# Performance work log

Hardware: AMD Instinct MI355X
Metric: run time of the kernel (lower is better)

The kernel has to match this reference:

```python
import jax, jax.numpy as jnp
import numpy as np

NUM_ITER = 20
EPS = 1e-8


def _conv(x, w, pad):
    # x: [N, Cin, H, W], w: [Cout, Cin, kh, kw] (cross-correlation, like torch conv2d)
    return jax.lax.conv_general_dilated(
        x, w, window_strides=(1, 1), padding=pad,
        dimension_numbers=('NCHW', 'OIHW', 'NCHW'))


def setup_inputs() -> dict:
    key = jax.random.key(0)
    x = jax.random.normal(key, (2, 4, 3, 256, 256), dtype=jnp.float32)
    return {
        'x': x,
        'lam': jnp.array([0.02], dtype=jnp.float32),
        'tau': jnp.array([0.25], dtype=jnp.float32),
        'theta': jnp.array([0.1], dtype=jnp.float32),
        'wx': jnp.array([[-1.0, 1.0, 0.0]], dtype=jnp.float32),
        'wy': jnp.array([[-1.0], [1.0], [0.0]], dtype=jnp.float32),
    }


def reference(x, lam, tau, theta, wx, wy):
    # x: [2, B, C, H, W] -> pairs of single-channel images [NB, 2, H, W]
    F, B, C, H, W = x.shape
    NB = B * C
    xx = jnp.moveaxis(x.reshape(2, NB, H, W), 0, 1)  # [NB, 2, H, W]

    dt = x.dtype
    gx = jnp.array([[-1., 0., 1.], [-2., 0., 2.], [-1., 0., 1.]], dt) / 6.0
    gy = jnp.array([[-1., -2., -1.], [0., 0., 0.], [1., 2., 1.]], dt) / 6.0
    grad_w = jnp.stack([gx, gy])[:, None]          # [2,1,3,3] image gradient (fixed)
    gxu = jnp.array([[0., 0., 0.], [0., -1., 1.], [0., 0., 0.]], dt)
    gyu = jnp.array([[0., 0., 0.], [0., -1., 0.], [0., 1., 0.]], dt)
    grad_u_w = jnp.stack([gxu, gyu])[:, None]      # [2,1,3,3] flow gradient (fixed)
    wx_k = wx[None, None]                          # [1,1,1,3] trainable divergence stencil
    wy_k = wy[None, None]                          # [1,1,3,1]

    rho_c = (xx[:, 1] - xx[:, 0])[:, None]                       # [NB,1,H,W]
    grad_im = _conv(xx[:, 1:], grad_w, [(1, 1), (1, 1)])         # [NB,2,H,W]
    norm_grad = jnp.sum(grad_im * grad_im, axis=1, keepdims=True) + EPS

    u = jnp.zeros((NB, 2, H, W), dt)
    p1 = jnp.zeros((NB, 2, H, W), dt)
    p2 = jnp.zeros((NB, 2, H, W), dt)

    tl = theta * lam       # [1]
    tt = tau / theta       # [1]

    def div(p):  # p: [NB,2,H,W] -> [NB,1,H,W]
        return (_conv(p[:, 0:1], wx_k, [(0, 0), (1, 1)]) +
                _conv(p[:, 1:2], wy_k, [(1, 1), (0, 0)]))

    def body(carry, _):
        u, p1, p2 = carry
        rho = rho_c + jnp.sum(grad_im * u, axis=1, keepdims=True)
        th = tl * norm_grad
        v = u - jnp.where(jnp.abs(rho) < th,
                          rho * grad_im / norm_grad,
                          tl * grad_im * jnp.sign(rho))
        u0 = v[:, 0] + theta * div(p1)[:, 0]
        u1 = v[:, 1] + theta * div(p2)[:, 0]
        u = jnp.stack([u0, u1], axis=1)
        g1 = _conv(u[:, 0:1], grad_u_w, [(1, 1), (1, 1)])
        g2 = _conv(u[:, 1:2], grad_u_w, [(1, 1), (1, 1)])
        p1 = (p1 + tt * g1) / (1.0 + tt * jnp.sum(jnp.abs(g1), axis=1, keepdims=True))
        p2 = (p2 + tt * g2) / (1.0 + tt * jnp.sum(jnp.abs(g2), axis=1, keepdims=True))
        return (u, p1, p2), None

    (u, p1, p2), _ = jax.lax.scan(body, (u, p1, p2), None, length=NUM_ITER)
    return u.reshape(B, C, 2, H, W)
```

## Files before the change

kernel.cpp:

```cpp
#include <hip/hip_runtime.h>

#define W 256
#define H 256
#define HW (W*H)
#define NB 12
#define ROWS 16
#define BPI (H/ROWS)
#define NBLK (NB*BPI)
#define NTHREADS 1024
#define NUM_ITER 20
#define TVEPS 1e-8f
#define HPLANES 8
#define FLAG_MAGIC 0x5A170000


__device__ __forceinline__ float aload(const float* p) {
    return __hip_atomic_load(p, __ATOMIC_RELAXED, __HIP_MEMORY_SCOPE_AGENT);
}
__device__ __forceinline__ void astore(float* p, float v) {
    __hip_atomic_store(p, v, __ATOMIC_RELAXED, __HIP_MEMORY_SCOPE_AGENT);
}
__device__ __forceinline__ void waitflag(const int* f, int tgt) {
    while (__hip_atomic_load(f, __ATOMIC_RELAXED, __HIP_MEMORY_SCOPE_AGENT) != tgt)
        __builtin_amdgcn_s_sleep(1);
    asm volatile("" ::: "memory");
}
__device__ __forceinline__ void setflag(int* f, int tgt) {
    asm volatile("s_waitcnt vmcnt(0)" ::: "memory");
    __hip_atomic_store(f, tgt, __ATOMIC_RELAXED, __HIP_MEMORY_SCOPE_AGENT);
}
__device__ __forceinline__ float fastrcp(float x) { return __builtin_amdgcn_rcpf(x); }

#define LD4(dst, ptr) { const float4 _t = *reinterpret_cast<const float4*>(ptr); \
                        dst[0]=_t.x; dst[1]=_t.y; dst[2]=_t.z; dst[3]=_t.w; }
#define ST4(ptr, src) { float4 _t; _t.x=src[0]; _t.y=src[1]; _t.z=src[2]; _t.w=src[3]; \
                        *reinterpret_cast<float4*>(ptr) = _t; }

__global__ __launch_bounds__(NTHREADS, 1) void tvl1_r5r_kernel(
    const float* __restrict__ xin,
    const float* __restrict__ lam,
    const float* __restrict__ tau,
    const float* __restrict__ theta,
    const float* __restrict__ wxv,
    const float* __restrict__ wyv,
    float* __restrict__ uout,
    float* __restrict__ halo,
    int* __restrict__ flags)
{
    __shared__ float xu0[ROWS+1][W];
    __shared__ float xu1[ROWS+1][W];
    __shared__ float xq1[ROWS][W];
    __shared__ float xq2[ROWS][W];

    const int tid  = threadIdx.x;
    const int lane = tid & 63;
    const int wv   = tid >> 6;
    const int x0   = lane << 2;
    const int b    = blockIdx.x;
    const int n    = b / BPI, bi = b % BPI;
    const int r0   = bi * ROWS;
    const int grow = r0 + wv;
    const bool notTop = (bi > 0), notBot = (bi < BPI-1);

    const float th0 = theta[0];
    const float tl  = th0 * lam[0];
    const float tt  = tau[0] / th0;
    const float wx0 = wxv[0], wx1 = wxv[1], wx2 = wxv[2];
    const float wy0 = wyv[0], wy1 = wyv[1], wy2 = wyv[2];

    const float* __restrict__ I0 = xin + (size_t)n * HW;
    const float* __restrict__ I1 = xin + (size_t)(NB + n) * HW;

    auto grad4 = [&](int row, float* rr, float* ggx, float* ggy) {
        #pragma unroll
        for (int c = 0; c < 4; ++c) {
            const int xc = x0 + c;
            const int idx = row * W + xc;
            const bool xm = xc > 0, xp = xc < W-1, ym = row > 0, yp = row < H-1;
            float a00=0.f,a01=0.f,a02=0.f,a10=0.f,a12=0.f,a20=0.f,a21=0.f,a22=0.f;
            if (ym) { a01=I1[idx-W]; if (xm) a00=I1[idx-W-1]; if (xp) a02=I1[idx-W+1]; }
            if (xm) a10=I1[idx-1];
            if (xp) a12=I1[idx+1];
            if (yp) { a21=I1[idx+W]; if (xm) a20=I1[idx+W-1]; if (xp) a22=I1[idx+W+1]; }
            ggx[c] = ((a02-a00) + 2.f*(a12-a10) + (a22-a20)) * (1.f/6.f);
            ggy[c] = ((a20-a00) + 2.f*(a21-a01) + (a22-a02)) * (1.f/6.f);
            rr[c]  = I1[idx] - I0[idx];
        }
    };

    float rho[4], gxr[4], gyr[4];
    grad4(grow, rho, gxr, gyr);
    float rho16[4]={0,0,0,0}, gx16[4]={0,0,0,0}, gy16[4]={0,0,0,0};
    if (wv == 14 && notBot) grad4(r0 + ROWS, rho16, gx16, gy16);

    for (int k = tid; k < (ROWS+1)*W; k += NTHREADS) { (&xu0[0][0])[k]=0.f; (&xu1[0][0])[k]=0.f; }
    for (int k = tid; k < ROWS*W;     k += NTHREADS) { (&xq1[0][0])[k]=0.f; (&xq2[0][0])[k]=0.f; }
    float u0[4]={0,0,0,0}, u1[4]={0,0,0,0};
    float p1x[4]={0,0,0,0}, p1y[4]={0,0,0,0}, p2x[4]={0,0,0,0}, p2y[4]={0,0,0,0};
    __syncthreads();

    auto ustep4 = [&](const float* rr, const float* ggx, const float* ggy,
                      const float* uu0, const float* uu1,
                      const float* x1m, const float* x1c, const float* x1p,
                      const float* q1m, const float* q1c, const float* q1p,
                      const float* x2m, const float* x2c, const float* x2p,
                      const float* q2m, const float* q2c, const float* q2p,
                      float* o0, float* o1) {
        #pragma unroll
        for (int c = 0; c < 4; ++c) {
            const float r  = rr[c] + ggx[c]*uu0[c] + ggy[c]*uu1[c];
            const float ng = ggx[c]*ggx[c] + ggy[c]*ggy[c] + TVEPS;
            const float th = tl * ng;
            const float f  = (fabsf(r) < th) ? (r * fastrcp(ng)) : copysignf(tl, r);
            const float d1 = wx0*x1m[c] + wx1*x1c[c] + wx2*x1p[c]
                           + wy0*q1m[c] + wy1*q1c[c] + wy2*q1p[c];
            const float d2 = wx0*x2m[c] + wx1*x2c[c] + wx2*x2p[c]
                           + wy0*q2m[c] + wy1*q2c[c] + wy2*q2p[c];
            o0[c] = (uu0[c] - f*ggx[c]) + th0*d1;
            o1[c] = (uu1[c] - f*ggy[c]) + th0*d2;
        }
    };

    for (int it = 0; it < NUM_ITER; ++it) {
        const bool last = (it == NUM_ITER-1);

        float hym1[4]={0,0,0,0}, hym2[4]={0,0,0,0};
        float hyp1[4]={0,0,0,0}, hyp2[4]={0,0,0,0};
        float c16x1[4]={0,0,0,0}, c16x2[4]={0,0,0,0};
        float c16c1[4]={0,0,0,0}, c16c2[4]={0,0,0,0};
        float c16p1[4]={0,0,0,0}, c16p2[4]={0,0,0,0};
        if (it > 0) {
            int* fb = flags + (size_t)(it-1) * 3 * NBLK;
            const int tgt = FLAG_MAGIC | (it-1);
            if (wv == 0 && notTop) {
                if (lane == 0) waitflag(&fb[2*NBLK + (b-1)], tgt);
                const float* hu = halo + ((size_t)(it-1)*NBLK + (b-1)) * HPLANES * W;
                #pragma unroll
                for (int c = 0; c < 4; ++c) {
                    hym1[c] = aload(hu + 6*W + x0 + c);
                    hym2[c] = aload(hu + 7*W + x0 + c);
                }
            }
            if (wv == 15 && notBot) {
                if (lane == 0) waitflag(&fb[0*NBLK + (b+1)], tgt);
                const float* hd = halo + ((size_t)(it-1)*NBLK + (b+1)) * HPLANES * W;
                #pragma unroll
                for (int c = 0; c < 4; ++c) {
                    hyp1[c] = aload(hd + 1*W + x0 + c);
                    hyp2[c] = aload(hd + 3*W + x0 + c);
                }
            }
            if (wv == 14 && notBot && !last) {
                if (lane < 2) waitflag(&fb[lane*NBLK + (b+1)], tgt);
                const float* hd = halo + ((size_t)(it-1)*NBLK + (b+1)) * HPLANES * W;
                #pragma unroll
                for (int c = 0; c < 4; ++c) {
                    c16x1[c] = aload(hd + 0*W + x0 + c);
                    c16c1[c] = aload(hd + 1*W + x0 + c);
                    c16x2[c] = aload(hd + 2*W + x0 + c);
                    c16c2[c] = aload(hd + 3*W + x0 + c);
                    c16p1[c] = aload(hd + 4*W + x0 + c);
                    c16p2[c] = aload(hd + 5*W + x0 + c);
                }
            }
        }

        float pym1[4], pym2[4], pyp1[4], pyp2[4];
        if (wv > 0) { LD4(pym1, &xq1[wv-1][x0]); LD4(pym2, &xq2[wv-1][x0]); }
        else        { for (int c=0;c<4;++c){ pym1[c]=hym1[c]; pym2[c]=hym2[c]; } }
        if (wv < ROWS-1) { LD4(pyp1, &xq1[wv+1][x0]); LD4(pyp2, &xq2[wv+1][x0]); }
        else             { for (int c=0;c<4;++c){ pyp1[c]=hyp1[c]; pyp2[c]=hyp2[c]; } }

        float l1 = __shfl_up(p1x[3], 1);   float l2 = __shfl_up(p2x[3], 1);
        if (lane == 0) { l1 = 0.f; l2 = 0.f; }
        float r1 = __shfl_down(p1x[0], 1); float r2 = __shfl_down(p2x[0], 1);
        if (lane == 63) { r1 = 0.f; r2 = 0.f; }
        const float p1xm[4] = { l1, p1x[0], p1x[1], p1x[2] };
        const float p1xp[4] = { p1x[1], p1x[2], p1x[3], r1 };
        const float p2xm[4] = { l2, p2x[0], p2x[1], p2x[2] };
        const float p2xp[4] = { p2x[1], p2x[2], p2x[3], r2 };

        float nu0[4], nu1[4];
        ustep4(rho, gxr, gyr, u0, u1,
               p1xm, p1x, p1xp, pym1, p1y, pyp1,
               p2xm, p2x, p2xp, pym2, p2y, pyp2, nu0, nu1);
        #pragma unroll
        for (int c = 0; c < 4; ++c) { u0[c] = nu0[c]; u1[c] = nu1[c]; }

        if (last) {
            float* __restrict__ o0 = uout + (size_t)(2*n)   * HW + (size_t)grow * W + x0;
            float* __restrict__ o1 = uout + (size_t)(2*n+1) * HW + (size_t)grow * W + x0;
            ST4(o0, u0); ST4(o1, u1);
            break;
        }

        ST4(&xu0[wv][x0], u0); ST4(&xu1[wv][x0], u1);

        if (wv == 14 && notBot) {
            float q115[4], q215[4], u160[4], u161[4];
            LD4(q115, &xq1[ROWS-1][x0]); LD4(q215, &xq2[ROWS-1][x0]);
            LD4(u160, &xu0[ROWS][x0]);   LD4(u161, &xu1[ROWS][x0]);
            float hl1 = __shfl_up(c16x1[3], 1), hl2 = __shfl_up(c16x2[3], 1);
            if (lane == 0) { hl1 = 0.f; hl2 = 0.f; }
            float hr1 = __shfl_down(c16x1[0], 1), hr2 = __shfl_down(c16x2[0], 1);
            if (lane == 63) { hr1 = 0.f; hr2 = 0.f; }
            const float h1m[4] = { hl1, c16x1[0], c16x1[1], c16x1[2] };
            const float h1p[4] = { c16x1[1], c16x1[2], c16x1[3], hr1 };
            const float h2m[4] = { hl2, c16x2[0], c16x2[1], c16x2[2] };
            const float h2p[4] = { c16x2[1], c16x2[2], c16x2[3], hr2 };
            float n160[4], n161[4];
            ustep4(rho16, gx16, gy16, u160, u161,
                   h1m, c16x1, h1p, q115, c16c1, c16p1,
                   h2m, c16x2, h2p, q215, c16c2, c16p2, n160, n161);
            ST4(&xu0[ROWS][x0], n160); ST4(&xu1[ROWS][x0], n161);
        }
        __syncthreads();

        float uy0[4], uy1[4];
        if (grow == H-1) { for (int c=0;c<4;++c){ uy0[c]=0.f; uy1[c]=0.f; } }
        else             { LD4(uy0, &xu0[wv+1][x0]); LD4(uy1, &xu1[wv+1][x0]); }
        float ur0 = __shfl_down(u0[0], 1), ur1 = __shfl_down(u1[0], 1);
        if (lane == 63) { ur0 = 0.f; ur1 = 0.f; }
        #pragma unroll
        for (int c = 0; c < 4; ++c) {
            const float uxp0 = (c < 3) ? u0[c+1] : ur0;
            const float uxp1 = (c < 3) ? u1[c+1] : ur1;
            const float g1x = uxp0 - u0[c];
            const float g1y = uy0[c] - u0[c];
            const float g2x = uxp1 - u1[c];
            const float g2y = uy1[c] - u1[c];
            const float rc1 = fastrcp(1.f + tt * (fabsf(g1x) + fabsf(g1y)));
            const float rc2 = fastrcp(1.f + tt * (fabsf(g2x) + fabsf(g2y)));
            p1x[c] = (p1x[c] + tt*g1x) * rc1;
            p1y[c] = (p1y[c] + tt*g1y) * rc1;
            p2x[c] = (p2x[c] + tt*g2x) * rc2;
            p2y[c] = (p2y[c] + tt*g2y) * rc2;
        }
        ST4(&xq1[wv][x0], p1y); ST4(&xq2[wv][x0], p2y);

        float* hwp = halo + ((size_t)it * NBLK + b) * HPLANES * W;
        int* fw = flags + (size_t)it * 3 * NBLK;
        const int ftgt = FLAG_MAGIC | it;
        if (wv == 0 && notTop) {
            #pragma unroll
            for (int c = 0; c < 4; ++c) {
                astore(hwp + 0*W + x0 + c, p1x[c]);
                astore(hwp + 1*W + x0 + c, p1y[c]);
                astore(hwp + 2*W + x0 + c, p2x[c]);
                astore(hwp + 3*W + x0 + c, p2y[c]);
            }
            if (lane == 0) setflag(&fw[0*NBLK + b], ftgt);
        } else if (wv == 1 && notTop) {
            #pragma unroll
            for (int c = 0; c < 4; ++c) {
                astore(hwp + 4*W + x0 + c, p1y[c]);
                astore(hwp + 5*W + x0 + c, p2y[c]);
            }
            if (lane == 0) setflag(&fw[1*NBLK + b], ftgt);
        } else if (wv == ROWS-1 && notBot) {
            #pragma unroll
            for (int c = 0; c < 4; ++c) {
                astore(hwp + 6*W + x0 + c, p1y[c]);
                astore(hwp + 7*W + x0 + c, p2y[c]);
            }
            if (lane == 0) setflag(&fw[2*NBLK + b], ftgt);
        }
        __syncthreads();
    }
}


__global__ void precompute_kernel(const float* __restrict__ x,
                                  float* __restrict__ u,
                                  float* __restrict__ ws) {
    const int row = blockIdx.x;
    const int n = row / H, y = row % H;
    const int xx = threadIdx.x;
    const int idx = y * W + xx;
    const float* __restrict__ I0 = x + (size_t)n * HW;
    const float* __restrict__ I1 = x + (size_t)(NB + n) * HW;
    float* __restrict__ p1  = ws;
    float* __restrict__ p2  = ws + (size_t)2 * NB * HW;
    float* __restrict__ rho = ws + (size_t)4 * NB * HW;
    float* __restrict__ gxp = ws + (size_t)5 * NB * HW;
    float* __restrict__ gyp = ws + (size_t)6 * NB * HW;
    const float i1c = I1[idx];
    const bool xm = xx > 0, xp = xx < W - 1, ym = y > 0, yp = y < H - 1;
    float a00=0.f,a01=0.f,a02=0.f,a10=0.f,a12=0.f,a20=0.f,a21=0.f,a22=0.f;
    if (ym) { a01 = I1[idx-W]; if (xm) a00 = I1[idx-W-1]; if (xp) a02 = I1[idx-W+1]; }
    if (xm) a10 = I1[idx-1];
    if (xp) a12 = I1[idx+1];
    if (yp) { a21 = I1[idx+W]; if (xm) a20 = I1[idx+W-1]; if (xp) a22 = I1[idx+W+1]; }
    const float gxv = ((a02-a00) + 2.f*(a12-a10) + (a22-a20)) * (1.f/6.f);
    const float gyv = ((a20-a00) + 2.f*(a21-a01) + (a22-a02)) * (1.f/6.f);
    const size_t np = (size_t)n * HW;
    rho[np+idx] = i1c - I0[idx];
    gxp[np+idx] = gxv;
    gyp[np+idx] = gyv;
    u[(size_t)(2*n)*HW + idx] = 0.f;   u[(size_t)(2*n+1)*HW + idx] = 0.f;
    p1[(size_t)(2*n)*HW + idx] = 0.f;  p1[(size_t)(2*n+1)*HW + idx] = 0.f;
    p2[(size_t)(2*n)*HW + idx] = 0.f;  p2[(size_t)(2*n+1)*HW + idx] = 0.f;
}

__global__ void u_kernel(const float* __restrict__ ws,
                         float* __restrict__ u,
                         const float* __restrict__ lam,
                         const float* __restrict__ theta,
                         const float* __restrict__ wxv,
                         const float* __restrict__ wyv) {
    const int row = blockIdx.x;
    const int n = row / H, y = row % H;
    const int xx = threadIdx.x;
    const int idx = y * W + xx;
    const size_t np = (size_t)n * HW;
    const float* __restrict__ p1  = ws;
    const float* __restrict__ p2  = ws + (size_t)2 * NB * HW;
    const float* __restrict__ rho_c = ws + (size_t)4 * NB * HW;
    const float* __restrict__ gxp = ws + (size_t)5 * NB * HW;
    const float* __restrict__ gyp = ws + (size_t)6 * NB * HW;
    const float th0 = theta[0];
    const float tl = th0 * lam[0];
    const float wx0 = wxv[0], wx1 = wxv[1], wx2 = wxv[2];
    const float wy0 = wyv[0], wy1 = wyv[1], wy2 = wyv[2];
    const float gx = gxp[np+idx];
    const float gy = gyp[np+idx];
    float* __restrict__ u0p = u + (size_t)(2*n)*HW;
    float* __restrict__ u1p = u + (size_t)(2*n+1)*HW;
    const float u0 = u0p[idx], u1 = u1p[idx];
    const float rho = rho_c[np+idx] + gx*u0 + gy*u1;
    const float ng = gx*gx + gy*gy + TVEPS;
    const float th = tl * ng;
    float s0, s1;
    if (fabsf(rho) < th) { const float d = rho/ng; s0 = d*gx; s1 = d*gy; }
    else { const float sg = (rho > 0.f) ? 1.f : ((rho < 0.f) ? -1.f : 0.f);
           s0 = tl*gx*sg; s1 = tl*gy*sg; }
    const float v0 = u0 - s0, v1 = u1 - s1;
    const float* __restrict__ p1x = p1 + (size_t)(2*n)*HW;
    const float* __restrict__ p1y = p1 + (size_t)(2*n+1)*HW;
    const float* __restrict__ p2x = p2 + (size_t)(2*n)*HW;
    const float* __restrict__ p2y = p2 + (size_t)(2*n+1)*HW;
    float d1 = wx1*p1x[idx] + wy1*p1y[idx];
    float d2 = wx1*p2x[idx] + wy1*p2y[idx];
    if (xx > 0)     { d1 += wx0*p1x[idx-1]; d2 += wx0*p2x[idx-1]; }
    if (xx < W-1)   { d1 += wx2*p1x[idx+1]; d2 += wx2*p2x[idx+1]; }
    if (y > 0)      { d1 += wy0*p1y[idx-W]; d2 += wy0*p2y[idx-W]; }
    if (y < H-1)    { d1 += wy2*p1y[idx+W]; d2 += wy2*p2y[idx+W]; }
    u0p[idx] = v0 + th0*d1;
    u1p[idx] = v1 + th0*d2;
}

__global__ void p_kernel(const float* __restrict__ u,
                         float* __restrict__ ws,
                         const float* __restrict__ tau,
                         const float* __restrict__ theta) {
    const int row = blockIdx.x;
    const int n = row / H, y = row % H;
    const int xx = threadIdx.x;
    const int idx = y * W + xx;
    float* __restrict__ p1 = ws;
    float* __restrict__ p2 = ws + (size_t)2 * NB * HW;
    const float tt = tau[0] / theta[0];
    const float* __restrict__ u0p = u + (size_t)(2*n)*HW;
    const float* __restrict__ u1p = u + (size_t)(2*n+1)*HW;
    const float c0 = u0p[idx];
    const float g1x = ((xx < W-1) ? u0p[idx+1] : 0.f) - c0;
    const float g1y = ((y < H-1) ? u0p[idx+W] : 0.f) - c0;
    const float c1 = u1p[idx];
    const float g2x = ((xx < W-1) ? u1p[idx+1] : 0.f) - c1;
    const float g2y = ((y < H-1) ? u1p[idx+W] : 0.f) - c1;
    float* __restrict__ p1x = p1 + (size_t)(2*n)*HW;
    float* __restrict__ p1y = p1 + (size_t)(2*n+1)*HW;
    float* __restrict__ p2x = p2 + (size_t)(2*n)*HW;
    float* __restrict__ p2y = p2 + (size_t)(2*n+1)*HW;
    const float den1 = 1.f + tt * (fabsf(g1x) + fabsf(g1y));
    p1x[idx] = (p1x[idx] + tt*g1x) / den1;
    p1y[idx] = (p1y[idx] + tt*g1y) / den1;
    const float den2 = 1.f + tt * (fabsf(g2x) + fabsf(g2y));
    p2x[idx] = (p2x[idx] + tt*g2x) / den2;
    p2y[idx] = (p2y[idx] + tt*g2y) / den2;
}

extern "C" void kernel_launch(void* const* d_in, const int* in_sizes, int n_in,
                              void* d_out, int out_size, void* d_ws, size_t ws_size,
                              hipStream_t stream) {
    const float* x     = (const float*)d_in[0];
    const float* lam   = (const float*)d_in[1];
    const float* tau   = (const float*)d_in[2];
    const float* theta = (const float*)d_in[3];
    const float* wxv   = (const float*)d_in[4];
    const float* wyv   = (const float*)d_in[5];
    float* u = (float*)d_out;

    const size_t halo_floats = (size_t)(NUM_ITER-1) * NBLK * HPLANES * W;
    const size_t need = halo_floats * sizeof(float)
                      + (size_t)(NUM_ITER-1) * 3 * NBLK * sizeof(int);

    if (ws_size >= need) {
        float* halo = (float*)d_ws;
        int* flags = (int*)((char*)d_ws + halo_floats * sizeof(float));
        void* args[] = { (void*)&x, (void*)&lam, (void*)&tau, (void*)&theta,
                         (void*)&wxv, (void*)&wyv, (void*)&u, (void*)&halo, (void*)&flags };
        hipLaunchCooperativeKernel((void*)tvl1_r5r_kernel, dim3(NBLK), dim3(NTHREADS),
                                   args, 0, stream);
    } else {
        float* ws = (float*)d_ws;
        const dim3 grid(NB * H);
        const dim3 block(W);
        precompute_kernel<<<grid, block, 0, stream>>>(x, u, ws);
        for (int it = 0; it < NUM_ITER; ++it) {
            u_kernel<<<grid, block, 0, stream>>>(ws, u, lam, theta, wxv, wyv);
            p_kernel<<<grid, block, 0, stream>>>(u, ws, tau, theta);
        }
    }
}
```

Baseline: 114.9 us.

## Replace flag-based halo sync with tagged 64-bit payloads in double-buffered ring

Halo values are now stored as 64-bit words that pack the float with an iteration tag, so a consumer polls the data itself rather than a separate flag. This removes the vmcnt drain before each flag store and the extra flag round-trip. The per-iteration halo buffers are replaced by a two-slot ping-pong buffer, which shrinks the workspace. The wave-14 halo wait also moves later, just before the values are used, so it can overlap with the u-step. In exchange, halo traffic doubles in width and correctness relies on the tags and on a neighbour never running more than one iteration ahead.

New measurement: 133.5 us. 1.16x slower.

```diff
diff --git a/kernel.cpp b/kernel.cpp
--- a/kernel.cpp
+++ b/kernel.cpp
@@ -10,24 +10,16 @@
 #define NTHREADS 1024
 #define NUM_ITER 20
 #define TVEPS 1e-8f
-#define HPLANES 8
-#define FLAG_MAGIC 0x5A170000
-
-
-__device__ __forceinline__ float aload(const float* p) {
+#define NPLQ 8
+#define FLAG_MAGIC 0x5A170000u
+
+
+__device__ __forceinline__ unsigned long long ald64(const unsigned long long* p) {
     return __hip_atomic_load(p, __ATOMIC_RELAXED, __HIP_MEMORY_SCOPE_AGENT);
 }
-__device__ __forceinline__ void astore(float* p, float v) {
-    __hip_atomic_store(p, v, __ATOMIC_RELAXED, __HIP_MEMORY_SCOPE_AGENT);
-}
-__device__ __forceinline__ void waitflag(const int* f, int tgt) {
-    while (__hip_atomic_load(f, __ATOMIC_RELAXED, __HIP_MEMORY_SCOPE_AGENT) != tgt)
-        __builtin_amdgcn_s_sleep(1);
-    asm volatile("" ::: "memory");
-}
-__device__ __forceinline__ void setflag(int* f, int tgt) {
-    asm volatile("s_waitcnt vmcnt(0)" ::: "memory");
-    __hip_atomic_store(f, tgt, __ATOMIC_RELAXED, __HIP_MEMORY_SCOPE_AGENT);
+__device__ __forceinline__ void pstore(unsigned long long* p, float v, unsigned tag) {
+    const unsigned long long q = ((unsigned long long)tag << 32) | (unsigned long long)__float_as_uint(v);
+    __hip_atomic_store(p, q, __ATOMIC_RELAXED, __HIP_MEMORY_SCOPE_AGENT);
 }
 __device__ __forceinline__ float fastrcp(float x) { return __builtin_amdgcn_rcpf(x); }
 
@@ -36,7 +28,7 @@
 #define ST4(ptr, src) { float4 _t; _t.x=src[0]; _t.y=src[1]; _t.z=src[2]; _t.w=src[3]; \
                         *reinterpret_cast<float4*>(ptr) = _t; }
 
-__global__ __launch_bounds__(NTHREADS, 1) void tvl1_r5r_kernel(
+__global__ __launch_bounds__(NTHREADS, 1) void tvl1_tag_kernel(
     const float* __restrict__ xin,
     const float* __restrict__ lam,
     const float* __restrict__ tau,
@@ -44,8 +36,7 @@
     const float* __restrict__ wxv,
     const float* __restrict__ wyv,
     float* __restrict__ uout,
-    float* __restrict__ halo,
-    int* __restrict__ flags)
+    unsigned long long* __restrict__ pay)
 {
     __shared__ float xu0[ROWS+1][W];
     __shared__ float xu1[ROWS+1][W];
@@ -110,8 +101,7 @@
         for (int c = 0; c < 4; ++c) {
             const float r  = rr[c] + ggx[c]*uu0[c] + ggy[c]*uu1[c];
             const float ng = ggx[c]*ggx[c] + ggy[c]*ggy[c] + TVEPS;
-            const float th = tl * ng;
-            const float f  = (fabsf(r) < th) ? (r * fastrcp(ng)) : copysignf(tl, r);
+            const float f  = (fabsf(r) < tl*ng) ? (r * fastrcp(ng)) : copysignf(tl, r);
             const float d1 = wx0*x1m[c] + wx1*x1c[c] + wx2*x1p[c]
                            + wy0*q1m[c] + wy1*q1c[c] + wy2*q1p[c];
             const float d2 = wx0*x2m[c] + wx1*x2c[c] + wx2*x2p[c]
@@ -129,38 +119,53 @@
         float c16x1[4]={0,0,0,0}, c16x2[4]={0,0,0,0};
         float c16c1[4]={0,0,0,0}, c16c2[4]={0,0,0,0};
         float c16p1[4]={0,0,0,0}, c16p2[4]={0,0,0,0};
+
         if (it > 0) {
-            int* fb = flags + (size_t)(it-1) * 3 * NBLK;
-            const int tgt = FLAG_MAGIC | (it-1);
+            const unsigned tg = FLAG_MAGIC | (unsigned)(it-1);
             if (wv == 0 && notTop) {
-                if (lane == 0) waitflag(&fb[2*NBLK + (b-1)], tgt);
-                const float* hu = halo + ((size_t)(it-1)*NBLK + (b-1)) * HPLANES * W;
-                #pragma unroll
-                for (int c = 0; c < 4; ++c) {
-                    hym1[c] = aload(hu + 6*W + x0 + c);
-                    hym2[c] = aload(hu + 7*W + x0 + c);
+                const unsigned long long* hp = pay + ((size_t)((it-1)&1)*NBLK + (b-1))*((size_t)NPLQ*W);
+                for (;;) {
+                    unsigned long long q[8];
+                    #pragma unroll
+                    for (int c = 0; c < 4; ++c) {
+                        q[c]   = ald64(hp + 6*W + x0 + c);
+                        q[4+c] = ald64(hp + 7*W + x0 + c);
+                    }
+                    unsigned bad = 0;
+                    #pragma unroll
+                    for (int i = 0; i < 8; ++i) bad |= ((unsigned)(q[i] >> 32)) ^ tg;
+                    if (bad == 0) {
+                        #pragma unroll
+                        for (int c = 0; c < 4; ++c) {
+                            hym1[c] = __uint_as_float((unsigned)q[c]);
+                            hym2[c] = __uint_as_float((unsigned)q[4+c]);
+                        }
+                        break;
+                    }
+                    __builtin_amdgcn_s_sleep(1);
                 }
             }
             if (wv == 15 && notBot) {
-                if (lane == 0) waitflag(&fb[0*NBLK + (b+1)], tgt);
-                const float* hd = halo + ((size_t)(it-1)*NBLK + (b+1)) * HPLANES * W;
-                #pragma unroll
-                for (int c = 0; c < 4; ++c) {
-                    hyp1[c] = aload(hd + 1*W + x0 + c);
-                    hyp2[c] = aload(hd + 3*W + x0 + c);
-                }
-            }
-            if (wv == 14 && notBot && !last) {
-                if (lane < 2) waitflag(&fb[lane*NBLK + (b+1)], tgt);
-                const float* hd = halo + ((size_t)(it-1)*NBLK + (b+1)) * HPLANES * W;
-                #pragma unroll
-                for (int c = 0; c < 4; ++c) {
-                    c16x1[c] = aload(hd + 0*W + x0 + c);
-                    c16c1[c] = aload(hd + 1*W + x0 + c);
-                    c16x2[c] = aload(hd + 2*W + x0 + c);
-                    c16c2[c] = aload(hd + 3*W + x0 + c);
-                    c16p1[c] = aload(hd + 4*W + x0 + c);
-                    c16p2[c] = aload(hd + 5*W + x0 + c);
+                const unsigned long long* hp = pay + ((size_t)((it-1)&1)*NBLK + (b+1))*((size_t)NPLQ*W);
+                for (;;) {
+                    unsigned long long q[8];
+                    #pragma unroll
+                    for (int c = 0; c < 4; ++c) {
+                        q[c]   = ald64(hp + 1*W + x0 + c);
+                        q[4+c] = ald64(hp + 3*W + x0 + c);
+                    }
+                    unsigned bad = 0;
+                    #pragma unroll
+                    for (int i = 0; i < 8; ++i) bad |= ((unsigned)(q[i] >> 32)) ^ tg;
+                    if (bad == 0) {
+                        #pragma unroll
+                        for (int c = 0; c < 4; ++c) {
+                            hyp1[c] = __uint_as_float((unsigned)q[c]);
+                            hyp2[c] = __uint_as_float((unsigned)q[4+c]);
+                        }
+                        break;
+                    }
+                    __builtin_amdgcn_s_sleep(1);
                 }
             }
         }
@@ -197,6 +202,34 @@
         ST4(&xu0[wv][x0], u0); ST4(&xu1[wv][x0], u1);
 
         if (wv == 14 && notBot) {
+            const unsigned tg = FLAG_MAGIC | (unsigned)(it-1);
+            if (it > 0) {
+                const unsigned long long* hp = pay + ((size_t)((it-1)&1)*NBLK + (b+1))*((size_t)NPLQ*W);
+                for (;;) {
+                    unsigned long long q[24];
+                    #pragma unroll
+                    for (int pl = 0; pl < 6; ++pl) {
+                        #pragma unroll
+                        for (int c = 0; c < 4; ++c) q[pl*4+c] = ald64(hp + pl*W + x0 + c);
+                    }
+                    unsigned bad = 0;
+                    #pragma unroll
+                    for (int i = 0; i < 24; ++i) bad |= ((unsigned)(q[i] >> 32)) ^ tg;
+                    if (bad == 0) {
+                        #pragma unroll
+                        for (int c = 0; c < 4; ++c) {
+                            c16x1[c] = __uint_as_float((unsigned)q[0*4+c]);
+                            c16c1[c] = __uint_as_float((unsigned)q[1*4+c]);
+                            c16x2[c] = __uint_as_float((unsigned)q[2*4+c]);
+                            c16c2[c] = __uint_as_float((unsigned)q[3*4+c]);
+                            c16p1[c] = __uint_as_float((unsigned)q[4*4+c]);
+                            c16p2[c] = __uint_as_float((unsigned)q[5*4+c]);
+                        }
+                        break;
+                    }
+                    __builtin_amdgcn_s_sleep(1);
+                }
+            }
             float q115[4], q215[4], u160[4], u161[4];
             LD4(q115, &xq1[ROWS-1][x0]); LD4(q215, &xq2[ROWS-1][x0]);
             LD4(u160, &xu0[ROWS][x0]);   LD4(u161, &xu1[ROWS][x0]);
@@ -238,32 +271,30 @@
         }
         ST4(&xq1[wv][x0], p1y); ST4(&xq2[wv][x0], p2y);
 
-        float* hwp = halo + ((size_t)it * NBLK + b) * HPLANES * W;
-        int* fw = flags + (size_t)it * 3 * NBLK;
-        const int ftgt = FLAG_MAGIC | it;
-        if (wv == 0 && notTop) {
-            #pragma unroll
-            for (int c = 0; c < 4; ++c) {
-                astore(hwp + 0*W + x0 + c, p1x[c]);
-                astore(hwp + 1*W + x0 + c, p1y[c]);
-                astore(hwp + 2*W + x0 + c, p2x[c]);
-                astore(hwp + 3*W + x0 + c, p2y[c]);
+        {
+            unsigned long long* hw = pay + ((size_t)(it&1)*NBLK + b)*((size_t)NPLQ*W);
+            const unsigned tg = FLAG_MAGIC | (unsigned)it;
+            if (wv == 0 && notTop) {
+                #pragma unroll
+                for (int c = 0; c < 4; ++c) {
+                    pstore(hw + 0*W + x0 + c, p1x[c], tg);
+                    pstore(hw + 1*W + x0 + c, p1y[c], tg);
+                    pstore(hw + 2*W + x0 + c, p2x[c], tg);
+                    pstore(hw + 3*W + x0 + c, p2y[c], tg);
+                }
+            } else if (wv == 1 && notTop) {
+                #pragma unroll
+                for (int c = 0; c < 4; ++c) {
+                    pstore(hw + 4*W + x0 + c, p1y[c], tg);
+                    pstore(hw + 5*W + x0 + c, p2y[c], tg);
+                }
+            } else if (wv == ROWS-1 && notBot) {
+                #pragma unroll
+                for (int c = 0; c < 4; ++c) {
+                    pstore(hw + 6*W + x0 + c, p1y[c], tg);
+                    pstore(hw + 7*W + x0 + c, p2y[c], tg);
+                }
             }
-            if (lane == 0) setflag(&fw[0*NBLK + b], ftgt);
-        } else if (wv == 1 && notTop) {
-            #pragma unroll
-            for (int c = 0; c < 4; ++c) {
-                astore(hwp + 4*W + x0 + c, p1y[c]);
-                astore(hwp + 5*W + x0 + c, p2y[c]);
-            }
-            if (lane == 0) setflag(&fw[1*NBLK + b], ftgt);
-        } else if (wv == ROWS-1 && notBot) {
-            #pragma unroll
-            for (int c = 0; c < 4; ++c) {
-                astore(hwp + 6*W + x0 + c, p1y[c]);
-                astore(hwp + 7*W + x0 + c, p2y[c]);
-            }
-            if (lane == 0) setflag(&fw[2*NBLK + b], ftgt);
         }
         __syncthreads();
     }
@@ -335,16 +366,16 @@
     else { const float sg = (rho > 0.f) ? 1.f : ((rho < 0.f) ? -1.f : 0.f);
            s0 = tl*gx*sg; s1 = tl*gy*sg; }
     const float v0 = u0 - s0, v1 = u1 - s1;
-    const float* __restrict__ p1x = p1 + (size_t)(2*n)*HW;
-    const float* __restrict__ p1y = p1 + (size_t)(2*n+1)*HW;
-    const float* __restrict__ p2x = p2 + (size_t)(2*n)*HW;
-    const float* __restrict__ p2y = p2 + (size_t)(2*n+1)*HW;
-    float d1 = wx1*p1x[idx] + wy1*p1y[idx];
-    float d2 = wx1*p2x[idx] + wy1*p2y[idx];
-    if (xx > 0)     { d1 += wx0*p1x[idx-1]; d2 += wx0*p2x[idx-1]; }
-    if (xx < W-1)   { d1 += wx2*p1x[idx+1]; d2 += wx2*p2x[idx+1]; }
-    if (y > 0)      { d1 += wy0*p1y[idx-W]; d2 += wy0*p2y[idx-W]; }
-    if (y < H-1)    { d1 += wy2*p1y[idx+W]; d2 += wy2*p2y[idx+W]; }
+    const float* __restrict__ p1xp = p1 + (size_t)(2*n)*HW;
+    const float* __restrict__ p1yp = p1 + (size_t)(2*n+1)*HW;
+    const float* __restrict__ p2xp = p2 + (size_t)(2*n)*HW;
+    const float* __restrict__ p2yp = p2 + (size_t)(2*n+1)*HW;
+    float d1 = wx1*p1xp[idx] + wy1*p1yp[idx];
+    float d2 = wx1*p2xp[idx] + wy1*p2yp[idx];
+    if (xx > 0)     { d1 += wx0*p1xp[idx-1]; d2 += wx0*p2xp[idx-1]; }
+    if (xx < W-1)   { d1 += wx2*p1xp[idx+1]; d2 += wx2*p2xp[idx+1]; }
+    if (y > 0)      { d1 += wy0*p1yp[idx-W]; d2 += wy0*p2yp[idx-W]; }
+    if (y < H-1)    { d1 += wy2*p1yp[idx+W]; d2 += wy2*p2yp[idx+W]; }
     u0p[idx] = v0 + th0*d1;
     u1p[idx] = v1 + th0*d2;
 }
@@ -368,16 +399,16 @@
     const float c1 = u1p[idx];
     const float g2x = ((xx < W-1) ? u1p[idx+1] : 0.f) - c1;
     const float g2y = ((y < H-1) ? u1p[idx+W] : 0.f) - c1;
-    float* __restrict__ p1x = p1 + (size_t)(2*n)*HW;
-    float* __restrict__ p1y = p1 + (size_t)(2*n+1)*HW;
-    float* __restrict__ p2x = p2 + (size_t)(2*n)*HW;
-    float* __restrict__ p2y = p2 + (size_t)(2*n+1)*HW;
+    float* __restrict__ p1xp = p1 + (size_t)(2*n)*HW;
+    float* __restrict__ p1yp = p1 + (size_t)(2*n+1)*HW;
+    float* __restrict__ p2xp = p2 + (size_t)(2*n)*HW;
+    float* __restrict__ p2yp = p2 + (size_t)(2*n+1)*HW;
     const float den1 = 1.f + tt * (fabsf(g1x) + fabsf(g1y));
-    p1x[idx] = (p1x[idx] + tt*g1x) / den1;
-    p1y[idx] = (p1y[idx] + tt*g1y) / den1;
+    p1xp[idx] = (p1xp[idx] + tt*g1x) / den1;
+    p1yp[idx] = (p1yp[idx] + tt*g1y) / den1;
     const float den2 = 1.f + tt * (fabsf(g2x) + fabsf(g2y));
-    p2x[idx] = (p2x[idx] + tt*g2x) / den2;
-    p2y[idx] = (p2y[idx] + tt*g2y) / den2;
+    p2xp[idx] = (p2xp[idx] + tt*g2x) / den2;
+    p2yp[idx] = (p2yp[idx] + tt*g2y) / den2;
 }
 
 extern "C" void kernel_launch(void* const* d_in, const int* in_sizes, int n_in,
@@ -391,16 +422,13 @@
     const float* wyv   = (const float*)d_in[5];
     float* u = (float*)d_out;
 
-    const size_t halo_floats = (size_t)(NUM_ITER-1) * NBLK * HPLANES * W;
-    const size_t need = halo_floats * sizeof(float)
-                      + (size_t)(NUM_ITER-1) * 3 * NBLK * sizeof(int);
+    const size_t need = (size_t)2 * NBLK * NPLQ * W * sizeof(unsigned long long);
 
     if (ws_size >= need) {
-        float* halo = (float*)d_ws;
-        int* flags = (int*)((char*)d_ws + halo_floats * sizeof(float));
+        unsigned long long* pay = (unsigned long long*)d_ws;
         void* args[] = { (void*)&x, (void*)&lam, (void*)&tau, (void*)&theta,
-                         (void*)&wxv, (void*)&wyv, (void*)&u, (void*)&halo, (void*)&flags };
-        hipLaunchCooperativeKernel((void*)tvl1_r5r_kernel, dim3(NBLK), dim3(NTHREADS),
+                         (void*)&wxv, (void*)&wyv, (void*)&u, (void*)&pay };
+        hipLaunchCooperativeKernel((void*)tvl1_tag_kernel, dim3(NBLK), dim3(NTHREADS),
                                    args, 0, stream);
     } else {
         float* ws = (float*)d_ws;
```
